# Optimization experiments

Measured on AMD Instinct MI355X. Metric: run time of the kernel, lower is better.

The kernel has to match this reference:

```python
import jax, jax.numpy as jnp
import numpy as np

N0, N1, N2 = 400000, 75000, 15000
E1, E2 = 1200000, 240000
F_IN, NC = 64, 40
H1, C1 = 2, 8          # layer 1: heads=2, out_channels=8 -> concat dim 16
H2, C2 = 1, NC         # layer 2: heads=1, out_channels=num_classes
NEG_SLOPE = 0.2


def gat_conv(x_src, x_dst, src, dst, Ws, Wd, att_s, att_d, bias, heads, ch):
    """PyG GATConv on bipartite (x_src, x_dst) with remove+add self loops."""
    n_dst = x_dst.shape[0]
    hs = (x_src @ Ws).reshape(-1, heads, ch)   # [N_src, H, C]
    hd = (x_dst @ Wd).reshape(-1, heads, ch)   # [N_dst, H, C]
    a_s = (hs * att_s).sum(-1)                 # [N_src, H]
    a_d = (hd * att_d).sum(-1)                 # [N_dst, H]
    loops = jnp.arange(n_dst)
    src_all = jnp.concatenate([src, loops])
    dst_all = jnp.concatenate([dst, loops])
    # remove_self_loops: drop pre-existing i->i edges; add_self_loops: appended
    valid = jnp.concatenate([src != dst, jnp.ones(n_dst, dtype=bool)])[:, None]
    logits = jax.nn.leaky_relu(a_s[src_all] + a_d[dst_all], NEG_SLOPE)  # [E, H]
    logits = jnp.where(valid, logits, -jnp.inf)
    m = jax.ops.segment_max(logits, dst_all, num_segments=n_dst)        # [N_dst, H]
    w = jnp.where(valid, jnp.exp(logits - m[dst_all]), 0.0)
    denom = jax.ops.segment_sum(w, dst_all, num_segments=n_dst)
    alpha = w / denom[dst_all]                                          # [E, H]
    out = jax.ops.segment_sum(alpha[:, :, None] * hs[src_all], dst_all,
                              num_segments=n_dst)                       # [N_dst, H, C]
    return out.reshape(n_dst, heads * ch) + bias


def setup_inputs() -> dict:
    key = jax.random.key(0)
    ks = jax.random.split(key, 16)
    s = 0.1
    return {
        "x": jax.random.normal(ks[0], (N0, F_IN), dtype=jnp.float32),
        "e1_src": jax.random.randint(ks[1], (E1,), 0, N0),
        "e1_dst": jax.random.randint(ks[2], (E1,), 0, N1),
        "e2_src": jax.random.randint(ks[3], (E2,), 0, N1),
        "e2_dst": jax.random.randint(ks[4], (E2,), 0, N2),
        "W1s": jax.random.normal(ks[5], (F_IN, H1 * C1), dtype=jnp.float32) * s,
        "W1d": jax.random.normal(ks[6], (F_IN, H1 * C1), dtype=jnp.float32) * s,
        "att1_s": jax.random.normal(ks[7], (H1, C1), dtype=jnp.float32) * s,
        "att1_d": jax.random.normal(ks[8], (H1, C1), dtype=jnp.float32) * s,
        "b1": jnp.zeros((H1 * C1,), dtype=jnp.float32),
        "W2s": jax.random.normal(ks[9], (H1 * C1, H2 * C2), dtype=jnp.float32) * s,
        "W2d": jax.random.normal(ks[10], (H1 * C1, H2 * C2), dtype=jnp.float32) * s,
        "att2_s": jax.random.normal(ks[11], (H2, C2), dtype=jnp.float32) * s,
        "att2_d": jax.random.normal(ks[12], (H2, C2), dtype=jnp.float32) * s,
        "b2": jnp.zeros((H2 * C2,), dtype=jnp.float32),
    }


def reference(x, e1_src, e1_dst, e2_src, e2_dst,
              W1s, W1d, att1_s, att1_d, b1,
              W2s, W2d, att2_s, att2_d, b2):
    h = gat_conv(x, x[:N1], e1_src, e1_dst, W1s, W1d, att1_s, att1_d, b1, H1, C1)
    h = jax.nn.elu(h)
    o = gat_conv(h, h[:N2], e2_src, e2_dst, W2s, W2d, att2_s, att2_d, b2, H2, C2)
    return jax.nn.log_softmax(o, axis=-1)
```

## Files before the change

kernel.cpp:

```cpp
#include <hip/hip_runtime.h>
#include <hip/hip_bf16.h>

constexpr int N0 = 400000, N1 = 75000, N2 = 15000;
constexpr int E1 = 1200000, E2 = 240000;
constexpr int NC = 40;
constexpr float NEG_SLOPE = 0.2f;

constexpr int BK1 = 128;
constexpr int NB1 = (N1 + BK1 - 1) / BK1;
constexpr int CAPB1 = 2432;
constexpr int BK2 = 32;
constexpr int NB2 = (N2 + BK2 - 1) / BK2;
constexpr int CAPB2 = 704;

constexpr int TILE = 4096;
constexpr int NT1L = (E1 + TILE - 1) / TILE;
constexpr int NT2L = (E2 + TILE - 1) / TILE;
constexpr int NTB = NT1L + NT2L;
constexpr int SUBCAP = 32;
constexpr int BPJ = N0 / 128;

using f32x4 = __attribute__((ext_vector_type(4))) float;
using s16x8 = __attribute__((ext_vector_type(8))) short;

__device__ __forceinline__ float leaky(float v) { return v > 0.f ? v : NEG_SLOPE * v; }

__device__ __forceinline__ unsigned cvtpk(float lo, float hi) {
    unsigned r;
    asm("v_cvt_pk_bf16_f32 %0, %1, %2" : "=v"(r) : "v"(lo), "v"(hi));
    return r;
}

__device__ __forceinline__ unsigned bf16pair(float lo, float hi) {
    unsigned a = __float_as_uint(lo), b = __float_as_uint(hi);
    a = (a + 0x7FFFu + ((a >> 16) & 1u)) >> 16;
    b = (b + 0x7FFFu + ((b >> 16) & 1u)) & 0xFFFF0000u;
    return a | b;
}
__device__ __forceinline__ float bfLo(unsigned w) { return __uint_as_float(w << 16); }
__device__ __forceinline__ float bfHi(unsigned w) { return __uint_as_float(w & 0xFFFF0000u); }

__global__ __launch_bounds__(256) void k1_kernel(
    const float* __restrict__ x,
    const float* __restrict__ W1s, const float* __restrict__ W1d,
    const float* __restrict__ att1s, const float* __restrict__ att1d,
    const int* __restrict__ e1s, const int* __restrict__ e1d,
    const int* __restrict__ e2s, const int* __restrict__ e2d,
    unsigned* __restrict__ rec1, float* __restrict__ a_d1,
    int* __restrict__ gcnt1, unsigned* __restrict__ bin1,
    int* __restrict__ gcnt2, unsigned* __restrict__ bin2)
{
    __shared__ int cur[NB1];
    __shared__ float2 vds[64];

    int bid = blockIdx.x;
    const int tid = threadIdx.x;
    if (bid < NTB) {
        const bool isL1 = bid < NT1L;
        const int t = isL1 ? bid : bid - NT1L;
        const int* es = isL1 ? e1s : e2s;
        const int* ed = isL1 ? e1d : e2d;
        const int nE = isL1 ? E1 : E2;
        const int nb = isL1 ? NB1 : NB2;
        const int shift = isL1 ? 7 : 5;
        const int lsh = isL1 ? 19 : 17;
        int* gc = isL1 ? gcnt1 : gcnt2;
        unsigned* gbin = isL1 ? bin1 : bin2;
        const int base = t * TILE;
        const int lim = min(TILE, nE - base);

        for (int b = tid; b < nb; b += 256) cur[b] = 0;
        __syncthreads();
        for (int i = tid; i < lim; i += 256) {
            int s = es[base + i], d = ed[base + i];
            if (s != d) {
                int b = d >> shift;
                int pos = atomicAdd(&cur[b], 1);
                if (pos < SUBCAP)
                    gbin[((size_t)t * nb + b) * SUBCAP + pos] =
                        (unsigned)s | ((unsigned)(d & ((1 << shift) - 1)) << lsh);
            }
        }
        __syncthreads();
        for (int b = tid; b < nb; b += 256)
            gc[(size_t)t * nb + b] = min(cur[b], SUBCAP);
        return;
    }
    bid -= NTB;
    const int l  = tid & 63;
    const int nd = l & 15;
    const int kg = l >> 4;
    const int wv = tid >> 6;
    const int nodeBase = bid * 128;
    const bool hasN1 = nodeBase < N1;

    if (hasN1) {
        if (tid < 64) {
            float d0 = 0.f, d1 = 0.f;
            const float* wr = W1d + (size_t)tid * 16;
            #pragma unroll
            for (int cc = 0; cc < 8; ++cc) {
                d0 = fmaf(wr[cc], att1d[cc], d0);
                d1 = fmaf(wr[8 + cc], att1d[8 + cc], d1);
            }
            vds[tid] = make_float2(d0, d1);
        }
        __syncthreads();
    }

    const int nodeA = nodeBase + wv * 32 + nd;
    const int nodeB = nodeA + 16;

    const float* xa = x + (size_t)nodeA * 64 + 8 * kg;
    const float* xb = x + (size_t)nodeB * 64 + 8 * kg;
    float4 qa0 = *(const float4*)(xa);
    float4 qa1 = *(const float4*)(xa + 4);
    float4 qa2 = *(const float4*)(xa + 32);
    float4 qa3 = *(const float4*)(xa + 36);
    float4 qb0 = *(const float4*)(xb);
    float4 qb1 = *(const float4*)(xb + 4);
    float4 qb2 = *(const float4*)(xb + 32);
    float4 qb3 = *(const float4*)(xb + 36);

    s16x8 bf0, bf1;
    {
        union { unsigned u[4]; s16x8 v; } t0, t1;
        #pragma unroll
        for (int q = 0; q < 4; ++q) {
            t0.u[q] = cvtpk(W1s[(8 * kg + 2 * q) * 16 + nd],
                            W1s[(8 * kg + 2 * q + 1) * 16 + nd]);
            t1.u[q] = cvtpk(W1s[(32 + 8 * kg + 2 * q) * 16 + nd],
                            W1s[(32 + 8 * kg + 2 * q + 1) * 16 + nd]);
        }
        bf0 = t0.v; bf1 = t1.v;
    }
    float att4[4];
    #pragma unroll
    for (int r = 0; r < 4; ++r) att4[r] = att1s[4 * kg + r];

    union { unsigned u[4]; s16x8 v; } a0, a1;
    a0.u[0] = cvtpk(qa0.x, qa0.y); a0.u[1] = cvtpk(qa0.z, qa0.w);
    a0.u[2] = cvtpk(qa1.x, qa1.y); a0.u[3] = cvtpk(qa1.z, qa1.w);
    a1.u[0] = cvtpk(qa2.x, qa2.y); a1.u[1] = cvtpk(qa2.z, qa2.w);
    a1.u[2] = cvtpk(qa3.x, qa3.y); a1.u[3] = cvtpk(qa3.z, qa3.w);
    f32x4 accA = {0.f, 0.f, 0.f, 0.f};
    accA = __builtin_amdgcn_mfma_f32_16x16x32_bf16(bf0, a0.v, accA, 0, 0, 0);
    accA = __builtin_amdgcn_mfma_f32_16x16x32_bf16(bf1, a1.v, accA, 0, 0, 0);

    union { unsigned u[4]; s16x8 v; } b0, b1;
    b0.u[0] = cvtpk(qb0.x, qb0.y); b0.u[1] = cvtpk(qb0.z, qb0.w);
    b0.u[2] = cvtpk(qb1.x, qb1.y); b0.u[3] = cvtpk(qb1.z, qb1.w);
    b1.u[0] = cvtpk(qb2.x, qb2.y); b1.u[1] = cvtpk(qb2.z, qb2.w);
    b1.u[2] = cvtpk(qb3.x, qb3.y); b1.u[3] = cvtpk(qb3.z, qb3.w);
    f32x4 accB = {0.f, 0.f, 0.f, 0.f};
    accB = __builtin_amdgcn_mfma_f32_16x16x32_bf16(bf0, b0.v, accB, 0, 0, 0);
    accB = __builtin_amdgcn_mfma_f32_16x16x32_bf16(bf1, b1.v, accB, 0, 0, 0);

    {
        float p = accA[0] * att4[0];
        p = fmaf(accA[1], att4[1], p);
        p = fmaf(accA[2], att4[2], p);
        p = fmaf(accA[3], att4[3], p);
        p += __shfl_xor(p, 16, 64);
        float q = __shfl_xor(p, 32, 64);
        unsigned* rp = rec1 + (size_t)nodeA * 16;
        uint2 hw; hw.x = cvtpk(accA[0], accA[1]); hw.y = cvtpk(accA[2], accA[3]);
        *(uint2*)(rp + 2 * kg) = hw;
        if (kg == 0)
            *(uint4*)(rp + 8) = make_uint4(__float_as_uint(p), __float_as_uint(q), 0u, 0u);
        else if (kg == 1)
            *(uint4*)(rp + 12) = make_uint4(0u, 0u, 0u, 0u);
    }
    {
        float p = accB[0] * att4[0];
        p = fmaf(accB[1], att4[1], p);
        p = fmaf(accB[2], att4[2], p);
        p = fmaf(accB[3], att4[3], p);
        p += __shfl_xor(p, 16, 64);
        float q = __shfl_xor(p, 32, 64);
        unsigned* rp = rec1 + (size_t)nodeB * 16;
        uint2 hw; hw.x = cvtpk(accB[0], accB[1]); hw.y = cvtpk(accB[2], accB[3]);
        *(uint2*)(rp + 2 * kg) = hw;
        if (kg == 0)
            *(uint4*)(rp + 8) = make_uint4(__float_as_uint(p), __float_as_uint(q), 0u, 0u);
        else if (kg == 1)
            *(uint4*)(rp + 12) = make_uint4(0u, 0u, 0u, 0u);
    }

    if (hasN1) {
        if (nodeA < N1) {
            float xv8[16] = {qa0.x, qa0.y, qa0.z, qa0.w, qa1.x, qa1.y, qa1.z, qa1.w,
                             qa2.x, qa2.y, qa2.z, qa2.w, qa3.x, qa3.y, qa3.z, qa3.w};
            float pd0 = 0.f, pd1 = 0.f;
            #pragma unroll
            for (int j = 0; j < 8; ++j) {
                float2 v = vds[8 * kg + j];
                pd0 = fmaf(xv8[j], v.x, pd0);
                pd1 = fmaf(xv8[j], v.y, pd1);
            }
            #pragma unroll
            for (int j = 0; j < 8; ++j) {
                float2 v = vds[32 + 8 * kg + j];
                pd0 = fmaf(xv8[8 + j], v.x, pd0);
                pd1 = fmaf(xv8[8 + j], v.y, pd1);
            }
            pd0 += __shfl_xor(pd0, 16, 64); pd0 += __shfl_xor(pd0, 32, 64);
            pd1 += __shfl_xor(pd1, 16, 64); pd1 += __shfl_xor(pd1, 32, 64);
            if (kg == 0) ((float2*)a_d1)[nodeA] = make_float2(pd0, pd1);
        }
        if (nodeB < N1) {
            float xv8[16] = {qb0.x, qb0.y, qb0.z, qb0.w, qb1.x, qb1.y, qb1.z, qb1.w,
                             qb2.x, qb2.y, qb2.z, qb2.w, qb3.x, qb3.y, qb3.z, qb3.w};
            float pd0 = 0.f, pd1 = 0.f;
            #pragma unroll
            for (int j = 0; j < 8; ++j) {
                float2 v = vds[8 * kg + j];
                pd0 = fmaf(xv8[j], v.x, pd0);
                pd1 = fmaf(xv8[j], v.y, pd1);
            }
            #pragma unroll
            for (int j = 0; j < 8; ++j) {
                float2 v = vds[32 + 8 * kg + j];
                pd0 = fmaf(xv8[8 + j], v.x, pd0);
                pd1 = fmaf(xv8[8 + j], v.y, pd1);
            }
            pd0 += __shfl_xor(pd0, 16, 64); pd0 += __shfl_xor(pd0, 32, 64);
            pd1 += __shfl_xor(pd1, 16, 64); pd1 += __shfl_xor(pd1, 32, 64);
            if (kg == 0) ((float2*)a_d1)[nodeB] = make_float2(pd0, pd1);
        }
    }
}

__global__ __launch_bounds__(1024) void k2_kernel(
    const int* __restrict__ gcnt1, const unsigned* __restrict__ bin1,
    const unsigned* __restrict__ rec1, const float* __restrict__ a_d1,
    const float* __restrict__ b1,
    const float* __restrict__ W2s, const float* __restrict__ W2d,
    const float* __restrict__ att2s, const float* __restrict__ att2d,
    unsigned* __restrict__ rec2)
{
    __shared__ unsigned raw[CAPB1];
    __shared__ unsigned srt[CAPB1];
    __shared__ int cnts[NT1L], pfx[NT1L + 1];
    __shared__ int hist[BK1], start[BK1 + 1];
    __shared__ float w2sl[640], va[16], vd[16];
    __shared__ float h1s[BK1][17];

    const int b = blockIdx.x, tid = threadIdx.x;
    const int d0 = b * BK1;
    const int nN = min(BK1, N1 - d0);

    for (int i = tid; i < 640; i += 1024) w2sl[i] = W2s[i];
    if (tid < BK1) hist[tid] = 0;
    if (tid >= 128 && tid < 144) {
        int k = tid - 128;
        float sa = 0.f, sd = 0.f;
        for (int cc = 0; cc < 40; ++cc) {
            sa = fmaf(W2s[k * 40 + cc], att2s[cc], sa);
            sd = fmaf(W2d[k * 40 + cc], att2d[cc], sd);
        }
        va[k] = sa; vd[k] = sd;
    }
    for (int i = tid; i < NT1L; i += 1024) cnts[i] = gcnt1[(size_t)i * NB1 + b];
    __syncthreads();
    if (tid < 64) {
        int carry = 0;
        #pragma unroll
        for (int s = 0; s < (NT1L + 63) / 64; ++s) {
            int idx = s * 64 + tid;
            int v = (idx < NT1L) ? cnts[idx] : 0;
            int xv = v;
            #pragma unroll
            for (int d = 1; d < 64; d <<= 1) {
                int t2 = __shfl_up(xv, d, 64);
                if (tid >= d) xv += t2;
            }
            if (idx < NT1L) pfx[idx] = carry + xv - v;
            carry += __shfl(xv, 63, 64);
        }
        if (tid == 0) pfx[NT1L] = carry;
    }
    __syncthreads();
    for (int j = tid; j < NT1L * SUBCAP; j += 1024) {
        int t = j >> 5, p = j & (SUBCAP - 1);
        if (p < cnts[t]) {
            int dst = pfx[t] + p;
            if (dst < CAPB1) {
                unsigned pay = bin1[((size_t)t * NB1 + b) * SUBCAP + p];
                raw[dst] = pay;
                atomicAdd(&hist[pay >> 19], 1);
            }
        }
    }
    __syncthreads();
    if (tid == 0) {
        int a = 0;
        for (int k = 0; k < BK1; ++k) { start[k] = a; a += hist[k]; }
        start[BK1] = a;
    }
    __syncthreads();
    if (tid < BK1) hist[tid] = start[tid];
    __syncthreads();
    const int total = min(pfx[NT1L], CAPB1);
    for (int i = tid; i < total; i += 1024) {
        unsigned p = raw[i];
        int pos = atomicAdd(&hist[p >> 19], 1);
        srt[pos] = p & 0x7FFFFu;
    }
    __syncthreads();

    const int g = tid >> 4, c = tid & 15, h = c >> 3;
    const int wbase = tid & 48;
    const int wmap = (c < 8) ? c : (8 + ((c >> 2) & 1));
    for (int n = g; n < nN; n += 64) {
        const int node = d0 + n;
        const float ad = a_d1[(size_t)node * 2 + h];
        const int st = start[n], cnt = start[n + 1] - start[n];
        unsigned rw0 = rec1[(size_t)node * 16 + wmap];
        unsigned rw1 = (cnt >= 1) ? rec1[(size_t)srt[st] * 16 + wmap] : 0u;
        unsigned rw2 = (cnt >= 2) ? rec1[(size_t)srt[st + 1] * 16 + wmap] : 0u;
        unsigned rw3 = (cnt >= 3) ? rec1[(size_t)srt[st + 2] * 16 + wmap] : 0u;
        float accv = 0.f, den = 0.f;
        for (int j = 0; j <= cnt; ++j) {
            float asv = __uint_as_float((unsigned)__shfl((int)rw0, wbase + 8 + 4 * h, 64));
            unsigned chw = (unsigned)__shfl((int)rw0, wbase + (c >> 1), 64);
            float hv = (c & 1) ? bfHi(chw) : bfLo(chw);
            float w = __expf(leaky(asv + ad));
            accv = fmaf(w, hv, accv);
            den += w;
            rw0 = rw1; rw1 = rw2; rw2 = rw3;
            rw3 = (j + 4 <= cnt) ? rec1[(size_t)srt[st + j + 3] * 16 + wmap] : 0u;
        }
        float v = accv / den + b1[c];
        h1s[n][c] = v > 0.f ? v : (__expf(v) - 1.f);
    }
    __syncthreads();
    for (int i = tid; i < nN * 24; i += 1024) {
        int nn = i / 24, w = i - nn * 24;
        unsigned* rp = rec2 + (size_t)(d0 + nn) * 24;
        if (w < 20) {
            int c0 = 2 * w, c1 = c0 + 1;
            float s0 = 0.f, s1 = 0.f;
            #pragma unroll
            for (int k = 0; k < 16; ++k) {
                float hk = h1s[nn][k];
                s0 = fmaf(hk, w2sl[k * 40 + c0], s0);
                s1 = fmaf(hk, w2sl[k * 40 + c1], s1);
            }
            rp[w] = bf16pair(s0, s1);
        } else if (w < 22) {
            const float* vv = (w == 20) ? va : vd;
            float s = 0.f;
            #pragma unroll
            for (int k = 0; k < 16; ++k) s = fmaf(h1s[nn][k], vv[k], s);
            rp[w] = __float_as_uint(s);
        }
    }
}

__global__ __launch_bounds__(1024) void k3_kernel(
    const int* __restrict__ gcnt2, const unsigned* __restrict__ bin2,
    const unsigned* __restrict__ rec2, const float* __restrict__ b2,
    float* __restrict__ out)
{
    __shared__ unsigned raw[CAPB2];
    __shared__ unsigned srt[CAPB2];
    __shared__ int cnts[NT2L], pfx[NT2L + 1];
    __shared__ int hist[BK2], start[BK2 + 1];

    const int b = blockIdx.x, tid = threadIdx.x;
    const int d0 = b * BK2;
    const int nN = min(BK2, N2 - d0);

    if (tid < BK2) hist[tid] = 0;
    if (tid < NT2L) cnts[tid] = gcnt2[(size_t)tid * NB2 + b];
    __syncthreads();
    if (tid < 64) {
        int v = (tid < NT2L) ? cnts[tid] : 0;
        int xv = v;
        #pragma unroll
        for (int d = 1; d < 64; d <<= 1) {
            int t2 = __shfl_up(xv, d, 64);
            if (tid >= d) xv += t2;
        }
        if (tid < NT2L) pfx[tid] = xv - v;
        if (tid == NT2L - 1) pfx[NT2L] = xv;
    }
    __syncthreads();
    for (int j = tid; j < NT2L * SUBCAP; j += 1024) {
        int t = j >> 5, p = j & (SUBCAP - 1);
        if (p < cnts[t]) {
            int dst = pfx[t] + p;
            if (dst < CAPB2) {
                unsigned pay = bin2[((size_t)t * NB2 + b) * SUBCAP + p];
                raw[dst] = pay;
                atomicAdd(&hist[pay >> 17], 1);
            }
        }
    }
    __syncthreads();
    if (tid == 0) {
        int a = 0;
        for (int k = 0; k < BK2; ++k) { start[k] = a; a += hist[k]; }
        start[BK2] = a;
    }
    __syncthreads();
    if (tid < BK2) hist[tid] = start[tid];
    __syncthreads();
    const int total = min(pfx[NT2L], CAPB2);
    for (int i = tid; i < total; i += 1024) {
        unsigned p = raw[i];
        int pos = atomicAdd(&hist[p >> 17], 1);
        srt[pos] = p & 0x1FFFFu;
    }
    __syncthreads();

    const int g = tid >> 5, l = tid & 31;
    const float bb0 = (l < 20) ? b2[2 * l] : 0.f;
    const float bb1 = (l < 20) ? b2[2 * l + 1] : 0.f;
    for (int n = g; n < nN; n += 32) {
        const int node = d0 + n;
        const int st = start[n], cnt = start[n + 1] - start[n];
        unsigned rw0 = (l < 22) ? rec2[(size_t)node * 24 + l] : 0u;
        const float ad = __uint_as_float((unsigned)__shfl((int)rw0, 21, 32));
        unsigned rw1 = (cnt >= 1 && l < 21) ? rec2[(size_t)srt[st] * 24 + l] : 0u;
        unsigned rw2 = (cnt >= 2 && l < 21) ? rec2[(size_t)srt[st + 1] * 24 + l] : 0u;
        unsigned rw3 = (cnt >= 3 && l < 21) ? rec2[(size_t)srt[st + 2] * 24 + l] : 0u;
        float a0 = 0.f, a1 = 0.f, den = 0.f;
        for (int j = 0; j <= cnt; ++j) {
            float asv = __uint_as_float((unsigned)__shfl((int)rw0, 20, 32));
            float w = __expf(leaky(asv + ad));
            a0 = fmaf(w, bfLo(rw0), a0);
            a1 = fmaf(w, bfHi(rw0), a1);
            den += w;
            rw0 = rw1; rw1 = rw2; rw2 = rw3;
            rw3 = (j + 4 <= cnt && l < 21) ? rec2[(size_t)srt[st + j + 3] * 24 + l] : 0u;
        }
        float v0 = (l < 20) ? a0 / den + bb0 : -3.4e38f;
        float v1 = (l < 20) ? a1 / den + bb1 : -3.4e38f;
        float mx = fmaxf(v0, v1);
        #pragma unroll
        for (int k = 16; k >= 1; k >>= 1) mx = fmaxf(mx, __shfl_xor(mx, k, 32));
        float ex = (l < 20) ? __expf(v0 - mx) + __expf(v1 - mx) : 0.f;
        #pragma unroll
        for (int k = 16; k >= 1; k >>= 1) ex += __shfl_xor(ex, k, 32);
        float lse = mx + logf(ex);
        if (l < 20)
            ((float2*)(out + (size_t)node * 40))[l] = make_float2(v0 - lse, v1 - lse);
    }
}

extern "C" void kernel_launch(void* const* d_in, const int* in_sizes, int n_in,
                              void* d_out, int out_size, void* d_ws, size_t ws_size,
                              hipStream_t stream) {
    const float* x      = (const float*)d_in[0];
    const int*   e1_src = (const int*)d_in[1];
    const int*   e1_dst = (const int*)d_in[2];
    const int*   e2_src = (const int*)d_in[3];
    const int*   e2_dst = (const int*)d_in[4];
    const float* W1s    = (const float*)d_in[5];
    const float* W1d    = (const float*)d_in[6];
    const float* att1s  = (const float*)d_in[7];
    const float* att1d  = (const float*)d_in[8];
    const float* b1     = (const float*)d_in[9];
    const float* W2s    = (const float*)d_in[10];
    const float* W2d    = (const float*)d_in[11];
    const float* att2s  = (const float*)d_in[12];
    const float* att2d  = (const float*)d_in[13];
    const float* b2     = (const float*)d_in[14];
    float* out = (float*)d_out;

    float* wsbase = (float*)d_ws;
    size_t o = 0;
    int*      gcnt1 = (int*)(wsbase + o);      o += (size_t)NT1L * NB1;
    int*      gcnt2 = (int*)(wsbase + o);      o += (size_t)NT2L * NB2;
    unsigned* bin1  = (unsigned*)(wsbase + o); o += (size_t)NT1L * NB1 * SUBCAP;
    unsigned* bin2  = (unsigned*)(wsbase + o); o += (size_t)NT2L * NB2 * SUBCAP;
    unsigned* rec1  = (unsigned*)(wsbase + o); o += (size_t)N0 * 16;
    float*    a_d1  = (float*)(wsbase + o);    o += (size_t)N1 * 2;
    unsigned* rec2  = (unsigned*)(wsbase + o); o += (size_t)N1 * 24;

    k1_kernel<<<NTB + BPJ, 256, 0, stream>>>(
        x, W1s, W1d, att1s, att1d, e1_src, e1_dst, e2_src, e2_dst,
        rec1, a_d1, gcnt1, bin1, gcnt2, bin2);

    k2_kernel<<<NB1, 1024, 0, stream>>>(gcnt1, bin1, rec1, a_d1, b1,
                                        W2s, W2d, att2s, att2d, rec2);

    k3_kernel<<<NB2, 1024, 0, stream>>>(gcnt2, bin2, rec2, b2, out);
}
```

Baseline: 124.9 us.

## Store layer-1 source features as fp8 with separate attention scores, shrink k2 blocks

Layer-1 projected source features move from bf16 in a padded 64-byte record to packed fp8 (16 bytes per node), and the source attention logits go to a separate float2 array. This cuts k1 write traffic and k2's random gather traffic. k2 now launches 512 threads per block and decodes fp8 when gathering. fp8 quantization adds accuracy risk to the aggregated features.

```diff
diff --git a/kernel.cpp b/kernel.cpp
--- a/kernel.cpp
+++ b/kernel.cpp
@@ -46,7 +46,7 @@
     const float* __restrict__ att1s, const float* __restrict__ att1d,
     const int* __restrict__ e1s, const int* __restrict__ e1d,
     const int* __restrict__ e2s, const int* __restrict__ e2d,
-    unsigned* __restrict__ rec1, float* __restrict__ a_d1,
+    unsigned* __restrict__ rec1, float* __restrict__ a_s1, float* __restrict__ a_d1,
     int* __restrict__ gcnt1, unsigned* __restrict__ bin1,
     int* __restrict__ gcnt2, unsigned* __restrict__ bin2)
 {
@@ -163,13 +163,10 @@
         p = fmaf(accA[3], att4[3], p);
         p += __shfl_xor(p, 16, 64);
         float q = __shfl_xor(p, 32, 64);
-        unsigned* rp = rec1 + (size_t)nodeA * 16;
-        uint2 hw; hw.x = cvtpk(accA[0], accA[1]); hw.y = cvtpk(accA[2], accA[3]);
-        *(uint2*)(rp + 2 * kg) = hw;
-        if (kg == 0)
-            *(uint4*)(rp + 8) = make_uint4(__float_as_uint(p), __float_as_uint(q), 0u, 0u);
-        else if (kg == 1)
-            *(uint4*)(rp + 12) = make_uint4(0u, 0u, 0u, 0u);
+        int w01 = __builtin_amdgcn_cvt_pk_fp8_f32(accA[0], accA[1], 0, false);
+        int w   = __builtin_amdgcn_cvt_pk_fp8_f32(accA[2], accA[3], w01, true);
+        rec1[(size_t)nodeA * 4 + kg] = (unsigned)w;
+        if (kg == 0) ((float2*)a_s1)[nodeA] = make_float2(p, q);
     }
     {
         float p = accB[0] * att4[0];
@@ -178,13 +175,10 @@
         p = fmaf(accB[3], att4[3], p);
         p += __shfl_xor(p, 16, 64);
         float q = __shfl_xor(p, 32, 64);
-        unsigned* rp = rec1 + (size_t)nodeB * 16;
-        uint2 hw; hw.x = cvtpk(accB[0], accB[1]); hw.y = cvtpk(accB[2], accB[3]);
-        *(uint2*)(rp + 2 * kg) = hw;
-        if (kg == 0)
-            *(uint4*)(rp + 8) = make_uint4(__float_as_uint(p), __float_as_uint(q), 0u, 0u);
-        else if (kg == 1)
-            *(uint4*)(rp + 12) = make_uint4(0u, 0u, 0u, 0u);
+        int w01 = __builtin_amdgcn_cvt_pk_fp8_f32(accB[0], accB[1], 0, false);
+        int w   = __builtin_amdgcn_cvt_pk_fp8_f32(accB[2], accB[3], w01, true);
+        rec1[(size_t)nodeB * 4 + kg] = (unsigned)w;
+        if (kg == 0) ((float2*)a_s1)[nodeB] = make_float2(p, q);
     }
 
     if (hasN1) {
@@ -231,10 +225,10 @@
     }
 }
 
-__global__ __launch_bounds__(1024) void k2_kernel(
+__global__ __launch_bounds__(512) void k2_kernel(
     const int* __restrict__ gcnt1, const unsigned* __restrict__ bin1,
-    const unsigned* __restrict__ rec1, const float* __restrict__ a_d1,
-    const float* __restrict__ b1,
+    const unsigned* __restrict__ rec1, const float* __restrict__ a_s1,
+    const float* __restrict__ a_d1, const float* __restrict__ b1,
     const float* __restrict__ W2s, const float* __restrict__ W2d,
     const float* __restrict__ att2s, const float* __restrict__ att2d,
     unsigned* __restrict__ rec2)
@@ -249,8 +243,9 @@
     const int b = blockIdx.x, tid = threadIdx.x;
     const int d0 = b * BK1;
     const int nN = min(BK1, N1 - d0);
-
-    for (int i = tid; i < 640; i += 1024) w2sl[i] = W2s[i];
+    const unsigned* a_s1w = (const unsigned*)a_s1;
+
+    for (int i = tid; i < 640; i += 512) w2sl[i] = W2s[i];
     if (tid < BK1) hist[tid] = 0;
     if (tid >= 128 && tid < 144) {
         int k = tid - 128;
@@ -261,7 +256,7 @@
         }
         va[k] = sa; vd[k] = sd;
     }
-    for (int i = tid; i < NT1L; i += 1024) cnts[i] = gcnt1[(size_t)i * NB1 + b];
+    for (int i = tid; i < NT1L; i += 512) cnts[i] = gcnt1[(size_t)i * NB1 + b];
     __syncthreads();
     if (tid < 64) {
         int carry = 0;
@@ -281,7 +276,7 @@
         if (tid == 0) pfx[NT1L] = carry;
     }
     __syncthreads();
-    for (int j = tid; j < NT1L * SUBCAP; j += 1024) {
+    for (int j = tid; j < NT1L * SUBCAP; j += 512) {
         int t = j >> 5, p = j & (SUBCAP - 1);
         if (p < cnts[t]) {
             int dst = pfx[t] + p;
@@ -302,7 +297,7 @@
     if (tid < BK1) hist[tid] = start[tid];
     __syncthreads();
     const int total = min(pfx[NT1L], CAPB1);
-    for (int i = tid; i < total; i += 1024) {
+    for (int i = tid; i < total; i += 512) {
         unsigned p = raw[i];
         int pos = atomicAdd(&hist[p >> 19], 1);
         srt[pos] = p & 0x7FFFFu;
@@ -311,31 +306,36 @@
 
     const int g = tid >> 4, c = tid & 15, h = c >> 3;
     const int wbase = tid & 48;
-    const int wmap = (c < 8) ? c : (8 + ((c >> 2) & 1));
-    for (int n = g; n < nN; n += 64) {
+    auto ldw = [&](int s) -> unsigned {
+        if (c < 4)  return rec1[(size_t)s * 4 + c];
+        if (c == 8)  return a_s1w[(size_t)s * 2];
+        if (c == 12) return a_s1w[(size_t)s * 2 + 1];
+        return 0u;
+    };
+    for (int n = g; n < nN; n += 32) {
         const int node = d0 + n;
         const float ad = a_d1[(size_t)node * 2 + h];
         const int st = start[n], cnt = start[n + 1] - start[n];
-        unsigned rw0 = rec1[(size_t)node * 16 + wmap];
-        unsigned rw1 = (cnt >= 1) ? rec1[(size_t)srt[st] * 16 + wmap] : 0u;
-        unsigned rw2 = (cnt >= 2) ? rec1[(size_t)srt[st + 1] * 16 + wmap] : 0u;
-        unsigned rw3 = (cnt >= 3) ? rec1[(size_t)srt[st + 2] * 16 + wmap] : 0u;
+        unsigned rw0 = ldw(node);
+        unsigned rw1 = (cnt >= 1) ? ldw(srt[st]) : 0u;
+        unsigned rw2 = (cnt >= 2) ? ldw(srt[st + 1]) : 0u;
+        unsigned rw3 = (cnt >= 3) ? ldw(srt[st + 2]) : 0u;
         float accv = 0.f, den = 0.f;
         for (int j = 0; j <= cnt; ++j) {
             float asv = __uint_as_float((unsigned)__shfl((int)rw0, wbase + 8 + 4 * h, 64));
-            unsigned chw = (unsigned)__shfl((int)rw0, wbase + (c >> 1), 64);
-            float hv = (c & 1) ? bfHi(chw) : bfLo(chw);
+            unsigned chw = (unsigned)__shfl((int)rw0, wbase + (c >> 2), 64);
+            float hv = __builtin_amdgcn_cvt_f32_fp8((int)(chw >> ((c & 3) * 8)), 0);
             float w = __expf(leaky(asv + ad));
             accv = fmaf(w, hv, accv);
             den += w;
             rw0 = rw1; rw1 = rw2; rw2 = rw3;
-            rw3 = (j + 4 <= cnt) ? rec1[(size_t)srt[st + j + 3] * 16 + wmap] : 0u;
+            rw3 = (j + 4 <= cnt) ? ldw(srt[st + j + 3]) : 0u;
         }
         float v = accv / den + b1[c];
         h1s[n][c] = v > 0.f ? v : (__expf(v) - 1.f);
     }
     __syncthreads();
-    for (int i = tid; i < nN * 24; i += 1024) {
+    for (int i = tid; i < nN * 24; i += 512) {
         int nn = i / 24, w = i - nn * 24;
         unsigned* rp = rec2 + (size_t)(d0 + nn) * 24;
         if (w < 20) {
@@ -476,16 +476,17 @@
     int*      gcnt2 = (int*)(wsbase + o);      o += (size_t)NT2L * NB2;
     unsigned* bin1  = (unsigned*)(wsbase + o); o += (size_t)NT1L * NB1 * SUBCAP;
     unsigned* bin2  = (unsigned*)(wsbase + o); o += (size_t)NT2L * NB2 * SUBCAP;
-    unsigned* rec1  = (unsigned*)(wsbase + o); o += (size_t)N0 * 16;
+    unsigned* rec1  = (unsigned*)(wsbase + o); o += (size_t)N0 * 4;
+    float*    a_s1  = (float*)(wsbase + o);    o += (size_t)N0 * 2;
     float*    a_d1  = (float*)(wsbase + o);    o += (size_t)N1 * 2;
     unsigned* rec2  = (unsigned*)(wsbase + o); o += (size_t)N1 * 24;
 
     k1_kernel<<<NTB + BPJ, 256, 0, stream>>>(
         x, W1s, W1d, att1s, att1d, e1_src, e1_dst, e2_src, e2_dst,
-        rec1, a_d1, gcnt1, bin1, gcnt2, bin2);
-
-    k2_kernel<<<NB1, 1024, 0, stream>>>(gcnt1, bin1, rec1, a_d1, b1,
-                                        W2s, W2d, att2s, att2d, rec2);
+        rec1, a_s1, a_d1, gcnt1, bin1, gcnt2, bin2);
+
+    k2_kernel<<<NB1, 512, 0, stream>>>(gcnt1, bin1, rec1, a_s1, a_d1, b1,
+                                       W2s, W2d, att2s, att2d, rec2);
 
     k3_kernel<<<NB2, 1024, 0, stream>>>(gcnt2, bin2, rec2, b2, out);
 }
```

Measured after the change: 160.1 us. 1.28x slower.

## Halve k2 block size and interleave four nodes per thread group in aggregation

Applied to the files above, without the earlier changes.

k2 now launches 512 threads per block. Each 16-lane group processes four destination nodes at once, interleaving their gather loops so several independent rec1 loads are in flight, with a prefetch depth of two per node instead of three. k1 gets an occupancy hint (launch_bounds 256,4) and a sched_barrier after the x loads to keep those loads issued early. The cost is more registers per thread and divergence when neighbour counts within a wave differ, since each group loops up to the largest of its four counts.

```diff
diff --git a/kernel.cpp b/kernel.cpp
--- a/kernel.cpp
+++ b/kernel.cpp
@@ -40,7 +40,7 @@
 __device__ __forceinline__ float bfLo(unsigned w) { return __uint_as_float(w << 16); }
 __device__ __forceinline__ float bfHi(unsigned w) { return __uint_as_float(w & 0xFFFF0000u); }
 
-__global__ __launch_bounds__(256) void k1_kernel(
+__global__ __launch_bounds__(256, 4) void k1_kernel(
     const float* __restrict__ x,
     const float* __restrict__ W1s, const float* __restrict__ W1d,
     const float* __restrict__ att1s, const float* __restrict__ att1d,
@@ -121,6 +121,7 @@
     float4 qb1 = *(const float4*)(xb + 4);
     float4 qb2 = *(const float4*)(xb + 32);
     float4 qb3 = *(const float4*)(xb + 36);
+    __builtin_amdgcn_sched_barrier(0);
 
     s16x8 bf0, bf1;
     {
@@ -231,7 +232,7 @@
     }
 }
 
-__global__ __launch_bounds__(1024) void k2_kernel(
+__global__ __launch_bounds__(512) void k2_kernel(
     const int* __restrict__ gcnt1, const unsigned* __restrict__ bin1,
     const unsigned* __restrict__ rec1, const float* __restrict__ a_d1,
     const float* __restrict__ b1,
@@ -250,7 +251,7 @@
     const int d0 = b * BK1;
     const int nN = min(BK1, N1 - d0);
 
-    for (int i = tid; i < 640; i += 1024) w2sl[i] = W2s[i];
+    for (int i = tid; i < 640; i += 512) w2sl[i] = W2s[i];
     if (tid < BK1) hist[tid] = 0;
     if (tid >= 128 && tid < 144) {
         int k = tid - 128;
@@ -261,7 +262,7 @@
         }
         va[k] = sa; vd[k] = sd;
     }
-    for (int i = tid; i < NT1L; i += 1024) cnts[i] = gcnt1[(size_t)i * NB1 + b];
+    for (int i = tid; i < NT1L; i += 512) cnts[i] = gcnt1[(size_t)i * NB1 + b];
     __syncthreads();
     if (tid < 64) {
         int carry = 0;
@@ -281,7 +282,7 @@
         if (tid == 0) pfx[NT1L] = carry;
     }
     __syncthreads();
-    for (int j = tid; j < NT1L * SUBCAP; j += 1024) {
+    for (int j = tid; j < NT1L * SUBCAP; j += 512) {
         int t = j >> 5, p = j & (SUBCAP - 1);
         if (p < cnts[t]) {
             int dst = pfx[t] + p;
@@ -302,7 +303,7 @@
     if (tid < BK1) hist[tid] = start[tid];
     __syncthreads();
     const int total = min(pfx[NT1L], CAPB1);
-    for (int i = tid; i < total; i += 1024) {
+    for (int i = tid; i < total; i += 512) {
         unsigned p = raw[i];
         int pos = atomicAdd(&hist[p >> 19], 1);
         srt[pos] = p & 0x7FFFFu;
@@ -312,30 +313,51 @@
     const int g = tid >> 4, c = tid & 15, h = c >> 3;
     const int wbase = tid & 48;
     const int wmap = (c < 8) ? c : (8 + ((c >> 2) & 1));
-    for (int n = g; n < nN; n += 64) {
-        const int node = d0 + n;
-        const float ad = a_d1[(size_t)node * 2 + h];
-        const int st = start[n], cnt = start[n + 1] - start[n];
-        unsigned rw0 = rec1[(size_t)node * 16 + wmap];
-        unsigned rw1 = (cnt >= 1) ? rec1[(size_t)srt[st] * 16 + wmap] : 0u;
-        unsigned rw2 = (cnt >= 2) ? rec1[(size_t)srt[st + 1] * 16 + wmap] : 0u;
-        unsigned rw3 = (cnt >= 3) ? rec1[(size_t)srt[st + 2] * 16 + wmap] : 0u;
-        float accv = 0.f, den = 0.f;
-        for (int j = 0; j <= cnt; ++j) {
-            float asv = __uint_as_float((unsigned)__shfl((int)rw0, wbase + 8 + 4 * h, 64));
-            unsigned chw = (unsigned)__shfl((int)rw0, wbase + (c >> 1), 64);
-            float hv = (c & 1) ? bfHi(chw) : bfLo(chw);
-            float w = __expf(leaky(asv + ad));
-            accv = fmaf(w, hv, accv);
-            den += w;
-            rw0 = rw1; rw1 = rw2; rw2 = rw3;
-            rw3 = (j + 4 <= cnt) ? rec1[(size_t)srt[st + j + 3] * 16 + wmap] : 0u;
-        }
-        float v = accv / den + b1[c];
-        h1s[n][c] = v > 0.f ? v : (__expf(v) - 1.f);
-    }
-    __syncthreads();
-    for (int i = tid; i < nN * 24; i += 1024) {
+    {
+        int   nI[4], stI[4], cnI[4];
+        float adI[4];
+        #pragma unroll
+        for (int q = 0; q < 4; ++q) {
+            int n = g + 32 * q;
+            bool v = n < nN;
+            nI[q]  = d0 + (v ? n : 0);
+            stI[q] = v ? start[n] : 0;
+            cnI[q] = v ? (start[n + 1] - stI[q]) : -1;
+            adI[q] = a_d1[(size_t)nI[q] * 2 + h];
+        }
+        unsigned rw0[4], rw1[4], rw2[4];
+        #pragma unroll
+        for (int q = 0; q < 4; ++q) {
+            rw0[q] = rec1[(size_t)nI[q] * 16 + wmap];
+            rw1[q] = (cnI[q] >= 1) ? rec1[(size_t)srt[stI[q]] * 16 + wmap] : 0u;
+            rw2[q] = (cnI[q] >= 2) ? rec1[(size_t)srt[stI[q] + 1] * 16 + wmap] : 0u;
+        }
+        float acc[4] = {0.f, 0.f, 0.f, 0.f}, den[4] = {0.f, 0.f, 0.f, 0.f};
+        const int mx = max(max(cnI[0], cnI[1]), max(cnI[2], cnI[3]));
+        for (int j = 0; j <= mx; ++j) {
+            #pragma unroll
+            for (int q = 0; q < 4; ++q) {
+                float asv = __uint_as_float((unsigned)__shfl((int)rw0[q], wbase + 8 + 4 * h, 64));
+                unsigned chw = (unsigned)__shfl((int)rw0[q], wbase + (c >> 1), 64);
+                float hv = (c & 1) ? bfHi(chw) : bfLo(chw);
+                float w = (j <= cnI[q]) ? __expf(leaky(asv + adI[q])) : 0.f;
+                acc[q] = fmaf(w, hv, acc[q]);
+                den[q] += w;
+                rw0[q] = rw1[q]; rw1[q] = rw2[q];
+                rw2[q] = (j + 3 <= cnI[q]) ? rec1[(size_t)srt[stI[q] + j + 2] * 16 + wmap] : 0u;
+            }
+        }
+        #pragma unroll
+        for (int q = 0; q < 4; ++q) {
+            int n = g + 32 * q;
+            if (n < nN) {
+                float v = acc[q] / den[q] + b1[c];
+                h1s[n][c] = v > 0.f ? v : (__expf(v) - 1.f);
+            }
+        }
+    }
+    __syncthreads();
+    for (int i = tid; i < nN * 24; i += 512) {
         int nn = i / 24, w = i - nn * 24;
         unsigned* rp = rec2 + (size_t)(d0 + nn) * 24;
         if (w < 20) {
@@ -484,8 +506,8 @@
         x, W1s, W1d, att1s, att1d, e1_src, e1_dst, e2_src, e2_dst,
         rec1, a_d1, gcnt1, bin1, gcnt2, bin2);
 
-    k2_kernel<<<NB1, 1024, 0, stream>>>(gcnt1, bin1, rec1, a_d1, b1,
-                                        W2s, W2d, att2s, att2d, rec2);
+    k2_kernel<<<NB1, 512, 0, stream>>>(gcnt1, bin1, rec1, a_d1, b1,
+                                       W2s, W2d, att2s, att2d, rec2);
 
     k3_kernel<<<NB2, 1024, 0, stream>>>(gcnt2, bin2, rec2, b2, out);
 }
```

Result: faster. 116.9 us (-6.4%).
